# Optimization experiments

Hardware: AMD Instinct MI355X
Metric: run time of the kernel (lower is better)

Reference implementation:

```python
import jax, jax.numpy as jnp
import numpy as np

B, K, C, H, W = 16, 512, 512, 64, 64

def setup_inputs() -> dict:
    key = jax.random.key(0)
    kx, kc = jax.random.split(key)
    x = jax.random.normal(kx, (B, C, H, W), dtype=jnp.float32)
    cluster_centers = jax.random.normal(kc, (1, K, C, 1, 1), dtype=jnp.float32)
    return {"x": x, "cluster_centers": cluster_centers}

def reference(x, cluster_centers):
    # Faithful to: torch.square(x[:, None] - centers).sum(2).argmin(1, keepdim=True)
    # Computed without the (B, K, C, H, W) broadcast intermediate via
    # and numerically the same distances up to fp rounding).
    c = cluster_centers[0, :, :, 0, 0]                      # (K, C)
    x_sq = jnp.sum(x * x, axis=1, keepdims=True)            # (B, 1, H, W)
    c_sq = jnp.sum(c * c, axis=1)[None, :, None, None]      # (1, K, 1, 1)
    cross = jnp.einsum('bchw,kc->bkhw', x, c)               # (B, K, H, W)
    dist = x_sq - 2.0 * cross + c_sq                        # (B, K, H, W)
    return jnp.argmin(dist, axis=1, keepdims=True)          # (B, 1, H, W) int
```

## Files before the change

### kernel.cpp

```cpp
#include <hip/hip_runtime.h>
#include <math.h>


#define NK   512
#define NC   512
#define NHW  4096
#define NPX  65536
#define MARGIN 0.05f

typedef unsigned short u16;
typedef __attribute__((ext_vector_type(8)))  _Float16 half8;
typedef __attribute__((ext_vector_type(8)))  unsigned short ushort8;
typedef __attribute__((ext_vector_type(16))) float  f32x16;

__device__ __forceinline__ u16 f2h(float f) {
    return __builtin_bit_cast(u16, (_Float16)f);
}

__global__ __launch_bounds__(64) void prep_pack(const float* __restrict__ cc,
                                                u16* __restrict__ wcc,
                                                float* __restrict__ shalf,
                                                double* __restrict__ csqd,
                                                int* __restrict__ gcnt) {
    const int k    = blockIdx.x;
    const int lane = threadIdx.x;
    if (k == 0 && lane == 0) gcnt[0] = 0;
    const int c0   = lane * 8;
    const float* row = cc + (size_t)k * NC + c0;
    ushort8 hi;
    double dsum = 0.0;
    #pragma unroll
    for (int i = 0; i < 8; ++i) {
        float v = row[i];
        dsum = fma((double)v, (double)v, dsum);
        hi[i] = f2h(v);
    }
    const int ch  = c0 >> 4;
    const int kh  = (c0 >> 3) & 1;
    const int mtg = k >> 5;
    const int h   = mtg >> 3;
    const int mtl = mtg & 7;
    const int ls  = (k & 31) + 32 * kh;
    *(ushort8*)(wcc + (((size_t)(ch * 2 + h) * 8 + mtl) * 64 + ls) * 8) = hi;
    #pragma unroll
    for (int off = 32; off > 0; off >>= 1) dsum += __shfl_down(dsum, off, 64);
    if (lane == 0) {
        csqd[k]  = dsum;
        shalf[k] = 0.5f * (float)dsum;
    }
}

__global__ __launch_bounds__(256) void transpose_cc(const float* __restrict__ cc,
                                                    float* __restrict__ cct) {
    __shared__ float tile[64][65];
    const int bi = blockIdx.x >> 3;
    const int bj = blockIdx.x & 7;
    const int tx = threadIdx.x & 63;
    const int ty = threadIdx.x >> 6;
    #pragma unroll
    for (int i = 0; i < 16; ++i) {
        const int r = ty + 4 * i;
        tile[r][tx] = cc[(size_t)(bi * 64 + r) * NC + bj * 64 + tx];
    }
    __syncthreads();
    #pragma unroll
    for (int i = 0; i < 16; ++i) {
        const int r = ty + 4 * i;
        cct[(size_t)(bj * 64 + r) * NK + bi * 64 + tx] = tile[tx][r];
    }
}

__global__ __launch_bounds__(256, 4) void codebook_mfma(
        const float* __restrict__ x,
        const u16* __restrict__ wcc,
        const float* __restrict__ shalf,
        float* __restrict__ cbv,
        float* __restrict__ csv,
        int*   __restrict__ ckk)
{
    __shared__ __align__(16) u16 cs0[8 * 512];
    __shared__ __align__(16) u16 cs1[8 * 512];
    __shared__ __align__(16) u16 xs0[2 * 512];
    __shared__ __align__(16) u16 xs1[2 * 512];

    const int tid  = threadIdx.x;
    const int w    = tid >> 6;
    const int lane = tid & 63;

    const int h   = blockIdx.x & 1;
    const int gp0 = (blockIdx.x >> 1) * 64;
    const float* xb = x + (size_t)(gp0 >> 12) * (NC * NHW) + (gp0 & (NHW - 1));

    f32x16 acc[2][2] = {};

    const int p   = tid & 63;
    const int xkh = w & 1;
    const int jq  = w >> 1;
    const int xoff = ((p >> 5) * 64 + ((p & 31) + 32 * xkh)) * 8 + jq * 4;
    const float* xp = xb + (size_t)(xkh * 8 + jq * 4) * NHW + p;

    float fxa[4], fxb[4];

    auto xload = [&](float* fx, int ch) {
        const float* xc = xp + (size_t)ch * 16 * NHW;
        fx[0] = xc[0];
        fx[1] = xc[NHW];
        fx[2] = xc[2 * NHW];
        fx[3] = xc[3 * NHW];
    };
    auto xwrite = [&](const float* fx, u16* xs) {
        u16 h0 = f2h(fx[0]), h1 = f2h(fx[1]), h2 = f2h(fx[2]), h3 = f2h(fx[3]);
        uint2 hv = make_uint2((unsigned)h0 | ((unsigned)h1 << 16),
                              (unsigned)h2 | ((unsigned)h3 << 16));
        *(uint2*)&xs[xoff] = hv;
    };
    auto stage_cs = [&](int ch, u16* dst) {
        #pragma unroll
        for (int i = 0; i < 2; ++i) {
            const int u = w * 2 + i;
            const u16* g = wcc + (((size_t)(ch * 2 + h) * 8 + u) * 64 + lane) * 8;
            __builtin_amdgcn_global_load_lds(
                (const __attribute__((address_space(1))) void*)g,
                (__attribute__((address_space(3))) void*)(dst + u * 512),
                16, 0, 0);
        }
    };
    auto compute = [&](const u16* csb, const u16* xsb) {
        __builtin_amdgcn_s_setprio(1);
        half8 bh[2];
        #pragma unroll
        for (int nt = 0; nt < 2; ++nt)
            bh[nt] = *(const half8*)&xsb[((size_t)nt * 64 + lane) * 8];
        #pragma unroll
        for (int mtl2 = 0; mtl2 < 2; ++mtl2) {
            const int gm = w * 2 + mtl2;
            half8 ah = *(const half8*)&csb[((size_t)gm * 64 + lane) * 8];
            #pragma unroll
            for (int nt = 0; nt < 2; ++nt)
                acc[mtl2][nt] = __builtin_amdgcn_mfma_f32_32x32x16_f16(ah, bh[nt], acc[mtl2][nt], 0, 0, 0);
        }
        __builtin_amdgcn_s_setprio(0);
    };

    auto phase = [&](int t, u16* cs_cur, u16* cs_nxt, u16* xs_cur, u16* xs_nxt,
                     float* fx_cur, float* fx_nxt) {
        stage_cs(t + 1, cs_nxt);
        __builtin_amdgcn_sched_barrier(0);
        xload(fx_nxt, t + 2);
        asm volatile("s_waitcnt vmcnt(6)" ::: "memory");
        xwrite(fx_cur, xs_nxt);
        compute(cs_cur, xs_cur);
        asm volatile("s_waitcnt vmcnt(4) lgkmcnt(0)" ::: "memory");
        __builtin_amdgcn_s_barrier();
        __builtin_amdgcn_sched_barrier(0);
    };

    xload(fxa, 0);
    __builtin_amdgcn_sched_barrier(0);
    stage_cs(0, cs0);
    __builtin_amdgcn_sched_barrier(0);
    xload(fxb, 1);
    asm volatile("s_waitcnt vmcnt(6)" ::: "memory");
    xwrite(fxa, xs0);
    asm volatile("s_waitcnt vmcnt(4) lgkmcnt(0)" ::: "memory");
    __builtin_amdgcn_s_barrier();
    __builtin_amdgcn_sched_barrier(0);

    for (int t = 0; t < 30; t += 2) {
        phase(t,     cs0, cs1, xs0, xs1, fxb, fxa);
        phase(t + 1, cs1, cs0, xs1, xs0, fxa, fxb);
    }

    stage_cs(31, cs1);
    asm volatile("s_waitcnt vmcnt(2)" ::: "memory");
    xwrite(fxb, xs1);
    compute(cs0, xs0);
    asm volatile("s_waitcnt vmcnt(0) lgkmcnt(0)" ::: "memory");
    __builtin_amdgcn_s_barrier();
    __builtin_amdgcn_sched_barrier(0);
    compute(cs1, xs1);
    __syncthreads();

    float* cand_v = (float*)cs0;
    float* cand_s = cand_v + 512;
    int*   cand_k = (int*)(cand_s + 512);
    float* sh_ep  = (float*)(cand_k + 512);

    sh_ep[tid] = shalf[h * 256 + tid];
    __syncthreads();

    const int qb = lane >> 5;
    #pragma unroll
    for (int nt = 0; nt < 2; ++nt) {
        float best = -INFINITY, sec = -INFINITY;
        int bk = 0;
        #pragma unroll
        for (int mtl2 = 0; mtl2 < 2; ++mtl2) {
            const int kbase = w * 64 + mtl2 * 32 + 4 * qb;
            #pragma unroll
            for (int reg = 0; reg < 16; ++reg) {
                const int k = kbase + (reg & 3) + 8 * (reg >> 2);
                const float v = acc[mtl2][nt][reg] - sh_ep[k];
                if (v > best) { sec = best; best = v; bk = k; }
                else if (v > sec) sec = v;
            }
        }
        const int pc   = nt * 32 + (lane & 31);
        const int slot = w * 2 + qb;
        cand_v[pc * 8 + slot] = best;
        cand_s[pc * 8 + slot] = sec;
        cand_k[pc * 8 + slot] = bk;
    }
    __syncthreads();

    if (tid < 64) {
        float best = -INFINITY, sec = -INFINITY;
        int bk = 1 << 30;
        #pragma unroll
        for (int s = 0; s < 8; ++s) {
            float v  = cand_v[tid * 8 + s];
            float v2 = cand_s[tid * 8 + s];
            int  kk  = cand_k[tid * 8 + s];
            if (v > best || (v == best && kk < bk)) {
                sec = fmaxf(sec, best);
                best = v; bk = kk;
            } else sec = fmaxf(sec, v);
            sec = fmaxf(sec, v2);
        }
        const int gpx = gp0 + tid;
        cbv[h * NPX + gpx] = best;
        csv[h * NPX + gpx] = sec;
        ckk[h * NPX + gpx] = h * 256 + bk;
    }
}

__global__ __launch_bounds__(256) void merge(
        const float* __restrict__ cbv,
        const float* __restrict__ csv,
        const int*   __restrict__ ckk,
        int* __restrict__ out,
        int* __restrict__ glist,
        int* __restrict__ gcnt)
{
    const int px = blockIdx.x * 256 + threadIdx.x;

    const float b0 = cbv[px],        b1 = cbv[NPX + px];
    const float s0 = csv[px],        s1 = csv[NPX + px];
    const int   k0 = ckk[px],        k1 = ckk[NPX + px];

    float best, sec; int bk;
    if (b0 >= b1) { best = b0; bk = k0; sec = fmaxf(s0, b1); }
    else          { best = b1; bk = k1; sec = fmaxf(s1, b0); }

    out[px] = bk;
    if (best - sec < MARGIN) {
        int i = atomicAdd(gcnt, 1);
        glist[i] = px;
    }
}

__global__ __launch_bounds__(256) void recheck(
        const float* __restrict__ x,
        const float* __restrict__ cct,
        const double* __restrict__ csqd,
        const int*   __restrict__ glist,
        const int*   __restrict__ gcnt,
        int* __restrict__ out)
{
    __shared__ float  xcol[2][NC];
    __shared__ double part[2][4][NK];
    __shared__ double dvv[256];
    __shared__ int    dii[256];

    const int tid  = threadIdx.x;
    const int w    = tid >> 6;
    const int lane = tid & 63;
    const int n    = gcnt[0];
    const int nb   = (n + 1) >> 1;

    for (int idx = blockIdx.x; idx < nb; idx += gridDim.x) {
        const int i0 = idx * 2;
        const int i1 = i0 + 1;
        const int px0 = glist[i0];
        const int px1 = (i1 < n) ? glist[i1] : px0;

        #pragma unroll
        for (int r = 0; r < 2; ++r) {
            const int c = tid + r * 256;
            xcol[0][c] = x[(size_t)(px0 >> 12) * (NC * NHW) + (size_t)c * NHW + (px0 & (NHW - 1))];
            xcol[1][c] = x[(size_t)(px1 >> 12) * (NC * NHW) + (size_t)c * NHW + (px1 & (NHW - 1))];
        }
        __syncthreads();

        double a0[8] = {}, a1[8] = {};
        const float4* cr = (const float4*)(cct + (size_t)(w * 128) * NK) + lane * 2;
        #pragma unroll 4
        for (int c0 = 0; c0 < 128; ++c0) {
            const float4 va = cr[0];
            const float4 vb = cr[1];
            cr += NK / 4;
            const double x0 = (double)xcol[0][w * 128 + c0];
            const double x1 = (double)xcol[1][w * 128 + c0];
            const double c4[8] = {(double)va.x, (double)va.y, (double)va.z, (double)va.w,
                                  (double)vb.x, (double)vb.y, (double)vb.z, (double)vb.w};
            #pragma unroll
            for (int j = 0; j < 8; ++j) {
                a0[j] = fma(x0, c4[j], a0[j]);
                a1[j] = fma(x1, c4[j], a1[j]);
            }
        }
        #pragma unroll
        for (int j = 0; j < 8; ++j) {
            part[0][w][lane * 8 + j] = a0[j];
            part[1][w][lane * 8 + j] = a1[j];
        }
        __syncthreads();

        #pragma unroll
        for (int pxi = 0; pxi < 2; ++pxi) {
            double bd = 1e300;
            int bkk = 1 << 30;
            #pragma unroll
            for (int r = 0; r < 2; ++r) {
                const int k = tid + r * 256;
                const double cross = part[pxi][0][k] + part[pxi][1][k]
                                   + part[pxi][2][k] + part[pxi][3][k];
                const double d = fma(-2.0, cross, csqd[k]);
                if (d < bd || (d == bd && k < bkk)) { bd = d; bkk = k; }
            }
            dvv[tid] = bd; dii[tid] = bkk;
            __syncthreads();
            for (int srd = 128; srd > 0; srd >>= 1) {
                if (tid < srd) {
                    double ov = dvv[tid + srd]; int oi = dii[tid + srd];
                    if (ov < dvv[tid] || (ov == dvv[tid] && oi < dii[tid])) {
                        dvv[tid] = ov; dii[tid] = oi;
                    }
                }
                __syncthreads();
            }
            if (tid == 0) out[pxi == 0 ? px0 : px1] = dii[0];
            __syncthreads();
        }
    }
}

extern "C" void kernel_launch(void* const* d_in, const int* in_sizes, int n_in,
                              void* d_out, int out_size, void* d_ws, size_t ws_size,
                              hipStream_t stream) {
    const float* x  = (const float*)d_in[0];
    const float* cc = (const float*)d_in[1];
    int* out = (int*)d_out;

    double* csqd  = (double*)d_ws;
    float*  shalf = (float*)(csqd + NK);
    u16*    wcc   = (u16*)(shalf + NK);
    float*  cct   = (float*)(wcc + 32 * 2 * 8 * 64 * 8);
    float*  cbv   = cct + (size_t)NC * NK;
    float*  csv   = cbv + 2 * NPX;
    int*    ckk   = (int*)(csv + 2 * NPX);
    int*    glist = ckk + 2 * NPX;
    int*    gcnt  = glist + NPX;

    prep_pack<<<NK, 64, 0, stream>>>(cc, wcc, shalf, csqd, gcnt);
    transpose_cc<<<64, 256, 0, stream>>>(cc, cct);
    codebook_mfma<<<(NPX / 64) * 2, 256, 0, stream>>>(x, wcc, shalf, cbv, csv, ckk);
    merge<<<NPX / 256, 256, 0, stream>>>(cbv, csv, ckk, out, glist, gcnt);
    recheck<<<1024, 256, 0, stream>>>(x, cct, csqd, glist, gcnt, out);
}
```

Measured before the change: 260.0 us.

## Fuse merge with recheck, fold transpose into prep, double codebook K-step

The codebook transpose moves into the prep kernel as a strided scatter, and the separate transpose kernel goes away. The merge and recheck kernels become one kernel in which each block merges 64 pixels and rechecks the ambiguous ones using a shared-memory list, so the global atomic counter and list are no longer needed. The MFMA main loop now stages two 16-channel chunks per phase, halving barrier and iteration count at the cost of double LDS use and more registers. This cuts launch and sync overhead, but the recheck work may be unevenly spread across blocks, and the scattered cct writes are uncoalesced.

```diff
diff --git a/kernel.cpp b/kernel.cpp
--- a/kernel.cpp
+++ b/kernel.cpp
@@ -21,10 +21,9 @@
                                                 u16* __restrict__ wcc,
                                                 float* __restrict__ shalf,
                                                 double* __restrict__ csqd,
-                                                int* __restrict__ gcnt) {
+                                                float* __restrict__ cct) {
     const int k    = blockIdx.x;
     const int lane = threadIdx.x;
-    if (k == 0 && lane == 0) gcnt[0] = 0;
     const int c0   = lane * 8;
     const float* row = cc + (size_t)k * NC + c0;
     ushort8 hi;
@@ -34,6 +33,7 @@
         float v = row[i];
         dsum = fma((double)v, (double)v, dsum);
         hi[i] = f2h(v);
+        cct[(size_t)(c0 + i) * NK + k] = v;
     }
     const int ch  = c0 >> 4;
     const int kh  = (c0 >> 3) & 1;
@@ -50,26 +50,6 @@
     }
 }
 
-__global__ __launch_bounds__(256) void transpose_cc(const float* __restrict__ cc,
-                                                    float* __restrict__ cct) {
-    __shared__ float tile[64][65];
-    const int bi = blockIdx.x >> 3;
-    const int bj = blockIdx.x & 7;
-    const int tx = threadIdx.x & 63;
-    const int ty = threadIdx.x >> 6;
-    #pragma unroll
-    for (int i = 0; i < 16; ++i) {
-        const int r = ty + 4 * i;
-        tile[r][tx] = cc[(size_t)(bi * 64 + r) * NC + bj * 64 + tx];
-    }
-    __syncthreads();
-    #pragma unroll
-    for (int i = 0; i < 16; ++i) {
-        const int r = ty + 4 * i;
-        cct[(size_t)(bj * 64 + r) * NK + bi * 64 + tx] = tile[tx][r];
-    }
-}
-
 __global__ __launch_bounds__(256, 4) void codebook_mfma(
         const float* __restrict__ x,
         const u16* __restrict__ wcc,
@@ -78,10 +58,10 @@
         float* __restrict__ csv,
         int*   __restrict__ ckk)
 {
-    __shared__ __align__(16) u16 cs0[8 * 512];
-    __shared__ __align__(16) u16 cs1[8 * 512];
-    __shared__ __align__(16) u16 xs0[2 * 512];
-    __shared__ __align__(16) u16 xs1[2 * 512];
+    __shared__ __align__(16) u16 cs0[16 * 512];
+    __shared__ __align__(16) u16 cs1[16 * 512];
+    __shared__ __align__(16) u16 xs0[4 * 512];
+    __shared__ __align__(16) u16 xs1[4 * 512];
 
     const int tid  = threadIdx.x;
     const int w    = tid >> 6;
@@ -99,45 +79,54 @@
     const int xoff = ((p >> 5) * 64 + ((p & 31) + 32 * xkh)) * 8 + jq * 4;
     const float* xp = xb + (size_t)(xkh * 8 + jq * 4) * NHW + p;
 
-    float fxa[4], fxb[4];
-
-    auto xload = [&](float* fx, int ch) {
-        const float* xc = xp + (size_t)ch * 16 * NHW;
-        fx[0] = xc[0];
-        fx[1] = xc[NHW];
-        fx[2] = xc[2 * NHW];
-        fx[3] = xc[3 * NHW];
+    float fxa[8], fxb[8];
+
+    auto xload = [&](float* fx, int sc) {
+        const float* xc0 = xp + (size_t)(2 * sc) * 16 * NHW;
+        const float* xc1 = xc0 + 16 * NHW;
+        fx[0] = xc0[0]; fx[1] = xc0[NHW]; fx[2] = xc0[2 * NHW]; fx[3] = xc0[3 * NHW];
+        fx[4] = xc1[0]; fx[5] = xc1[NHW]; fx[6] = xc1[2 * NHW]; fx[7] = xc1[3 * NHW];
     };
     auto xwrite = [&](const float* fx, u16* xs) {
-        u16 h0 = f2h(fx[0]), h1 = f2h(fx[1]), h2 = f2h(fx[2]), h3 = f2h(fx[3]);
-        uint2 hv = make_uint2((unsigned)h0 | ((unsigned)h1 << 16),
-                              (unsigned)h2 | ((unsigned)h3 << 16));
-        *(uint2*)&xs[xoff] = hv;
-    };
-    auto stage_cs = [&](int ch, u16* dst) {
-        #pragma unroll
-        for (int i = 0; i < 2; ++i) {
-            const int u = w * 2 + i;
-            const u16* g = wcc + (((size_t)(ch * 2 + h) * 8 + u) * 64 + lane) * 8;
-            __builtin_amdgcn_global_load_lds(
-                (const __attribute__((address_space(1))) void*)g,
-                (__attribute__((address_space(3))) void*)(dst + u * 512),
-                16, 0, 0);
+        #pragma unroll
+        for (int sub = 0; sub < 2; ++sub) {
+            u16 h0 = f2h(fx[sub * 4 + 0]), h1 = f2h(fx[sub * 4 + 1]);
+            u16 h2 = f2h(fx[sub * 4 + 2]), h3 = f2h(fx[sub * 4 + 3]);
+            uint2 hv = make_uint2((unsigned)h0 | ((unsigned)h1 << 16),
+                                  (unsigned)h2 | ((unsigned)h3 << 16));
+            *(uint2*)&xs[sub * 1024 + xoff] = hv;
+        }
+    };
+    auto stage_cs = [&](int sc, u16* dst) {
+        #pragma unroll
+        for (int sub = 0; sub < 2; ++sub) {
+            #pragma unroll
+            for (int i = 0; i < 2; ++i) {
+                const int u = w * 2 + i;
+                const u16* g = wcc + ((((size_t)(2 * sc + sub) * 2 + h) * 8 + u) * 64 + lane) * 8;
+                __builtin_amdgcn_global_load_lds(
+                    (const __attribute__((address_space(1))) void*)g,
+                    (__attribute__((address_space(3))) void*)(dst + (sub * 8 + u) * 512),
+                    16, 0, 0);
+            }
         }
     };
     auto compute = [&](const u16* csb, const u16* xsb) {
         __builtin_amdgcn_s_setprio(1);
-        half8 bh[2];
-        #pragma unroll
-        for (int nt = 0; nt < 2; ++nt)
-            bh[nt] = *(const half8*)&xsb[((size_t)nt * 64 + lane) * 8];
-        #pragma unroll
-        for (int mtl2 = 0; mtl2 < 2; ++mtl2) {
-            const int gm = w * 2 + mtl2;
-            half8 ah = *(const half8*)&csb[((size_t)gm * 64 + lane) * 8];
+        #pragma unroll
+        for (int sub = 0; sub < 2; ++sub) {
+            half8 bh[2];
             #pragma unroll
             for (int nt = 0; nt < 2; ++nt)
-                acc[mtl2][nt] = __builtin_amdgcn_mfma_f32_32x32x16_f16(ah, bh[nt], acc[mtl2][nt], 0, 0, 0);
+                bh[nt] = *(const half8*)&xsb[sub * 1024 + ((size_t)nt * 64 + lane) * 8];
+            #pragma unroll
+            for (int mtl2 = 0; mtl2 < 2; ++mtl2) {
+                const int gm = w * 2 + mtl2;
+                half8 ah = *(const half8*)&csb[((size_t)(sub * 8 + gm) * 64 + lane) * 8];
+                #pragma unroll
+                for (int nt = 0; nt < 2; ++nt)
+                    acc[mtl2][nt] = __builtin_amdgcn_mfma_f32_32x32x16_f16(ah, bh[nt], acc[mtl2][nt], 0, 0, 0);
+            }
         }
         __builtin_amdgcn_s_setprio(0);
     };
@@ -147,10 +136,10 @@
         stage_cs(t + 1, cs_nxt);
         __builtin_amdgcn_sched_barrier(0);
         xload(fx_nxt, t + 2);
-        asm volatile("s_waitcnt vmcnt(6)" ::: "memory");
+        asm volatile("s_waitcnt vmcnt(12)" ::: "memory");
         xwrite(fx_cur, xs_nxt);
         compute(cs_cur, xs_cur);
-        asm volatile("s_waitcnt vmcnt(4) lgkmcnt(0)" ::: "memory");
+        asm volatile("s_waitcnt vmcnt(8) lgkmcnt(0)" ::: "memory");
         __builtin_amdgcn_s_barrier();
         __builtin_amdgcn_sched_barrier(0);
     };
@@ -160,19 +149,19 @@
     stage_cs(0, cs0);
     __builtin_amdgcn_sched_barrier(0);
     xload(fxb, 1);
-    asm volatile("s_waitcnt vmcnt(6)" ::: "memory");
+    asm volatile("s_waitcnt vmcnt(12)" ::: "memory");
     xwrite(fxa, xs0);
-    asm volatile("s_waitcnt vmcnt(4) lgkmcnt(0)" ::: "memory");
+    asm volatile("s_waitcnt vmcnt(8) lgkmcnt(0)" ::: "memory");
     __builtin_amdgcn_s_barrier();
     __builtin_amdgcn_sched_barrier(0);
 
-    for (int t = 0; t < 30; t += 2) {
+    for (int t = 0; t < 14; t += 2) {
         phase(t,     cs0, cs1, xs0, xs1, fxb, fxa);
         phase(t + 1, cs1, cs0, xs1, xs0, fxa, fxb);
     }
 
-    stage_cs(31, cs1);
-    asm volatile("s_waitcnt vmcnt(2)" ::: "memory");
+    stage_cs(15, cs1);
+    asm volatile("s_waitcnt vmcnt(4)" ::: "memory");
     xwrite(fxb, xs1);
     compute(cs0, xs0);
     asm volatile("s_waitcnt vmcnt(0) lgkmcnt(0)" ::: "memory");
@@ -234,55 +223,47 @@
     }
 }
 
-__global__ __launch_bounds__(256) void merge(
+__global__ __launch_bounds__(256) void merge_recheck(
+        const float* __restrict__ x,
+        const float* __restrict__ cct,
+        const double* __restrict__ csqd,
         const float* __restrict__ cbv,
         const float* __restrict__ csv,
         const int*   __restrict__ ckk,
-        int* __restrict__ out,
-        int* __restrict__ glist,
-        int* __restrict__ gcnt)
-{
-    const int px = blockIdx.x * 256 + threadIdx.x;
-
-    const float b0 = cbv[px],        b1 = cbv[NPX + px];
-    const float s0 = csv[px],        s1 = csv[NPX + px];
-    const int   k0 = ckk[px],        k1 = ckk[NPX + px];
-
-    float best, sec; int bk;
-    if (b0 >= b1) { best = b0; bk = k0; sec = fmaxf(s0, b1); }
-    else          { best = b1; bk = k1; sec = fmaxf(s1, b0); }
-
-    out[px] = bk;
-    if (best - sec < MARGIN) {
-        int i = atomicAdd(gcnt, 1);
-        glist[i] = px;
-    }
-}
-
-__global__ __launch_bounds__(256) void recheck(
-        const float* __restrict__ x,
-        const float* __restrict__ cct,
-        const double* __restrict__ csqd,
-        const int*   __restrict__ glist,
-        const int*   __restrict__ gcnt,
         int* __restrict__ out)
 {
     __shared__ float  xcol[2][NC];
     __shared__ double part[2][4][NK];
     __shared__ double dvv[256];
     __shared__ int    dii[256];
+    __shared__ int    list[64];
+    __shared__ int    nflag;
 
     const int tid  = threadIdx.x;
     const int w    = tid >> 6;
     const int lane = tid & 63;
-    const int n    = gcnt[0];
-    const int nb   = (n + 1) >> 1;
-
-    for (int idx = blockIdx.x; idx < nb; idx += gridDim.x) {
-        const int i0 = idx * 2;
-        const int i1 = i0 + 1;
-        const int px0 = glist[i0];
-        const int px1 = (i1 < n) ? glist[i1] : px0;
+    const int pb   = blockIdx.x * 64;
+
+    if (tid == 0) nflag = 0;
+    __syncthreads();
+
+    if (tid < 64) {
+        const int px = pb + tid;
+        const float b0 = cbv[px], b1 = cbv[NPX + px];
+        const float s0 = csv[px], s1 = csv[NPX + px];
+        const int   k0 = ckk[px], k1 = ckk[NPX + px];
+        float best, sec; int bk;
+        if (b0 >= b1) { best = b0; bk = k0; sec = fmaxf(s0, b1); }
+        else          { best = b1; bk = k1; sec = fmaxf(s1, b0); }
+        out[px] = bk;
+        if (best - sec < MARGIN) { int i = atomicAdd(&nflag, 1); list[i] = px; }
+    }
+    __syncthreads();
+
+    const int n = nflag;
+    for (int idx = 0; idx < n; idx += 2) {
+        const int px0 = list[idx];
+        const int px1 = (idx + 1 < n) ? list[idx + 1] : px0;
 
         #pragma unroll
         for (int r = 0; r < 2; ++r) {
@@ -359,12 +340,8 @@
     float*  cbv   = cct + (size_t)NC * NK;
     float*  csv   = cbv + 2 * NPX;
     int*    ckk   = (int*)(csv + 2 * NPX);
-    int*    glist = ckk + 2 * NPX;
-    int*    gcnt  = glist + NPX;
-
-    prep_pack<<<NK, 64, 0, stream>>>(cc, wcc, shalf, csqd, gcnt);
-    transpose_cc<<<64, 256, 0, stream>>>(cc, cct);
+
+    prep_pack<<<NK, 64, 0, stream>>>(cc, wcc, shalf, csqd, cct);
     codebook_mfma<<<(NPX / 64) * 2, 256, 0, stream>>>(x, wcc, shalf, cbv, csv, ckk);
-    merge<<<NPX / 256, 256, 0, stream>>>(cbv, csv, ckk, out, glist, gcnt);
-    recheck<<<1024, 256, 0, stream>>>(x, cct, csqd, glist, gcnt, out);
-}
+    merge_recheck<<<NPX / 64, 256, 0, stream>>>(x, cct, csqd, cbv, csv, ckk, out);
+}
```

New measurement: 265.0 us. Within noise of the previous version (+1.9%).
